# Performance work log

Hardware: AMD Instinct MI355X
Metric: run time of the kernel (lower is better)

The kernel has to match this reference:

```python
import jax, jax.numpy as jnp
import numpy as np

V = 256       # num_variables
D = 512       # hidden_dim
B = 1024      # batch


def setup_inputs() -> dict:
    key = jax.random.key(0)
    ks = jax.random.split(key, 8)
    s1 = 1.0 / np.sqrt(V + 1)
    s2 = 1.0 / np.sqrt(D)
    return {
        "x": jax.random.normal(ks[0], (B, V), dtype=jnp.float32),
        "adjacency": jax.random.normal(ks[1], (V, V), dtype=jnp.float32),
        "W1": jax.random.normal(ks[2], (V, D, V + 1), dtype=jnp.float32) * s1,
        "b1": jax.random.normal(ks[3], (V, D), dtype=jnp.float32) * s1,
        "W2": jax.random.normal(ks[4], (V, D, D), dtype=jnp.float32) * s2,
        "b2": jax.random.normal(ks[5], (V, D), dtype=jnp.float32) * s2,
        "W3": jax.random.normal(ks[6], (V, D), dtype=jnp.float32) * s2,
        "b3": jax.random.normal(ks[7], (V,), dtype=jnp.float32) * s2,
    }


def reference(x, adjacency, W1, b1, W2, b2, W3, b3):
    # weighted_x[b, i] = (x @ A.T)[b, i]
    wx = x @ adjacency.T  # [B, V]
    # combined input for variable i: cat([x, wx[:, i:i+1]]) -> width V+1
    # build [B, V, V+1] by broadcasting x across the variable axis
    x_b = jnp.broadcast_to(x[:, None, :], (x.shape[0], V, V))
    comb = jnp.concatenate([x_b, wx[:, :, None]], axis=-1)  # [B, V, V+1]
    # per-variable 3-layer MLP, batched over the variable axis i
    h1 = jax.nn.relu(jnp.einsum('bij,idj->bid', comb, W1) + b1)   # [B, V, D]
    h2 = jax.nn.relu(jnp.einsum('bid,ied->bie', h1, W2) + b2)     # [B, V, D]
    out = jnp.einsum('bid,id->bi', h2, W3) + b3                   # [B, V]
    return out
```

## Files before the change

### kernel.cpp

```cpp
#include <hip/hip_runtime.h>
#include <hip/hip_bf16.h>
#include <stdint.h>

#define VNUM 256
#define DNUM 512
#define BNUM 1024

typedef __attribute__((ext_vector_type(8))) short bf16x8;
typedef __attribute__((ext_vector_type(4))) float f32x4;

__device__ __forceinline__ uint16_t f2bf(float f) {
    uint32_t u = __float_as_uint(f);
    uint32_t r = (u + 0x7FFFu + ((u >> 16) & 1u)) >> 16;
    return (uint16_t)r;
}

__device__ __forceinline__ void gl_lds16(const void* g, void* l) {
    __builtin_amdgcn_global_load_lds(
        (const __attribute__((address_space(1))) uint32_t*)g,
        (__attribute__((address_space(3))) uint32_t*)l, 16, 0, 0);
}

__global__ __launch_bounds__(256) void wx_kernel(const float* __restrict__ x,
                                                 const float* __restrict__ adj,
                                                 float* __restrict__ wx) {
    __shared__ float xs[64][36];
    __shared__ float as_[64][36];
    const int b0 = blockIdx.x * 64, i0 = blockIdx.y * 64;
    const int t = threadIdx.x;
    const int tx = t & 15, ty = t >> 4;
    const int lr = t >> 2, lk = (t & 3) * 8;
    float c[4][4] = {};
    for (int k0 = 0; k0 < 256; k0 += 32) {
        __syncthreads();
        *(float4*)&xs[lr][lk]      = *(const float4*)&x[(size_t)(b0 + lr) * VNUM + k0 + lk];
        *(float4*)&xs[lr][lk + 4]  = *(const float4*)&x[(size_t)(b0 + lr) * VNUM + k0 + lk + 4];
        *(float4*)&as_[lr][lk]     = *(const float4*)&adj[(size_t)(i0 + lr) * VNUM + k0 + lk];
        *(float4*)&as_[lr][lk + 4] = *(const float4*)&adj[(size_t)(i0 + lr) * VNUM + k0 + lk + 4];
        __syncthreads();
        #pragma unroll
        for (int kk = 0; kk < 32; kk++) {
            float xv[4], av[4];
            #pragma unroll
            for (int a = 0; a < 4; a++) xv[a] = xs[ty + a * 16][kk];
            #pragma unroll
            for (int b = 0; b < 4; b++) av[b] = as_[tx + b * 16][kk];
            #pragma unroll
            for (int a = 0; a < 4; a++)
                #pragma unroll
                for (int b = 0; b < 4; b++) c[a][b] += xv[a] * av[b];
        }
    }
    #pragma unroll
    for (int a = 0; a < 4; a++)
        #pragma unroll
        for (int b = 0; b < 4; b++)
            wx[(size_t)(b0 + ty + a * 16) * VNUM + i0 + tx + b * 16] = c[a][b];
}

__global__ __launch_bounds__(256) void xcvt_kernel(const float* __restrict__ x,
                                                   uint16_t* __restrict__ xbf) {
    const int idx = (blockIdx.x * 256 + threadIdx.x) * 4;
    float4 v = *(const float4*)&x[idx];
    uint32_t p0 = (uint32_t)f2bf(v.x) | ((uint32_t)f2bf(v.y) << 16);
    uint32_t p1 = (uint32_t)f2bf(v.z) | ((uint32_t)f2bf(v.w) << 16);
    *(uint2*)&xbf[idx] = make_uint2(p0, p1);
}

__global__ __launch_bounds__(256) void w1cvt_kernel(const float* __restrict__ W1,
                                                    uint16_t* __restrict__ W1bf,
                                                    float* __restrict__ w1last) {
    const size_t idx = (size_t)blockIdx.x * 256 + threadIdx.x;
    const size_t row = idx >> 8;
    const int    k   = (int)(idx & 255);
    const float* src = W1 + row * 257;
    W1bf[idx] = f2bf(src[k]);
    if (k == 0) w1last[row] = src[256];
}

__global__ __launch_bounds__(256) void w2cvt_kernel(const float* __restrict__ W2,
                                                    uint16_t* __restrict__ W2bf) {
    const size_t idx = ((size_t)blockIdx.x * 256 + threadIdx.x) * 4;
    float4 v = *(const float4*)&W2[idx];
    uint32_t p0 = (uint32_t)f2bf(v.x) | ((uint32_t)f2bf(v.y) << 16);
    uint32_t p1 = (uint32_t)f2bf(v.z) | ((uint32_t)f2bf(v.w) << 16);
    *(uint2*)&W2bf[idx] = make_uint2(p0, p1);
}

__global__ __launch_bounds__(256) void gemm1_kernel(const uint16_t* __restrict__ xbf,
                                                    const float* __restrict__ wx,
                                                    const uint16_t* __restrict__ W1bf,
                                                    const float* __restrict__ w1last,
                                                    const float* __restrict__ b1,
                                                    uint16_t* __restrict__ h1) {
    const int b0 = blockIdx.x * 128;
    const int d0 = blockIdx.y * 128;
    const int ci = blockIdx.z;
    const int i  = ci;

    __shared__ __align__(16) uint16_t As[128 * 32];
    __shared__ __align__(16) uint16_t Bs[128 * 32];
    __shared__ float wxs[128], w1ls[128], b1s[128];

    const int t = threadIdx.x;
    const int w = t >> 6, l = t & 63;
    const int wm = w >> 1, wn = w & 1;
    const int q = l >> 4, lo = l & 15;

    if (t < 128) {
        wxs[t] = wx[(size_t)(b0 + t) * VNUM + i];
        b1s[t] = b1[(size_t)i * DNUM + d0 + t];
    } else {
        int tt = t - 128;
        w1ls[tt] = w1last[(size_t)i * DNUM + d0 + tt];
    }

    f32x4 acc[4][4];
    #pragma unroll
    for (int a = 0; a < 4; a++)
        #pragma unroll
        for (int b = 0; b < 4; b++) { f32x4 z = {0.f, 0.f, 0.f, 0.f}; acc[a][b] = z; }

    const int c_  = w * 64 + l;
    const int rA  = c_ >> 2,        kA = (c_ & 3) ^ ((rA >> 2) & 0);

    const uint16_t* Abase = xbf;
    const uint16_t* Bbase = W1bf + (size_t)i * DNUM * 256;

    for (int k0 = 0; k0 < 256; k0 += 32) {
        __syncthreads();
        #pragma unroll
        for (int p = 0; p < 2; p++) {
            int c  = p * 256 + w * 64 + l;
            int r  = c >> 2, k2 = c & 3;
            int gk2 = k2 ^ ((r >> 1) & 3);
            gl_lds16(Abase + (size_t)(b0 + r) * 256 + k0 + gk2 * 8,
                     &As[(p * 256 + w * 64) * 8]);
        }
        #pragma unroll
        for (int p = 0; p < 2; p++) {
            int c  = p * 256 + w * 64 + l;
            int r  = c >> 2, k2 = c & 3;
            int gk2 = k2 ^ ((r >> 1) & 3);
            gl_lds16(Bbase + (size_t)(d0 + r) * 256 + k0 + gk2 * 8,
                     &Bs[(p * 256 + w * 64) * 8]);
        }
        __syncthreads();
        bf16x8 af[4], bfr[4];
        #pragma unroll
        for (int mt = 0; mt < 4; mt++) {
            int m = wm * 64 + mt * 16 + lo;
            int slot = q ^ ((m >> 1) & 3);
            af[mt] = *(const bf16x8*)&As[m * 32 + slot * 8];
        }
        #pragma unroll
        for (int nt = 0; nt < 4; nt++) {
            int n = wn * 64 + nt * 16 + lo;
            int slot = q ^ ((n >> 1) & 3);
            bfr[nt] = *(const bf16x8*)&Bs[n * 32 + slot * 8];
        }
        #pragma unroll
        for (int mt = 0; mt < 4; mt++)
            #pragma unroll
            for (int nt = 0; nt < 4; nt++)
                acc[mt][nt] = __builtin_amdgcn_mfma_f32_16x16x32_bf16(af[mt], bfr[nt], acc[mt][nt], 0, 0, 0);
    }
    (void)rA; (void)kA;

    #pragma unroll
    for (int mt = 0; mt < 4; mt++) {
        #pragma unroll
        for (int reg = 0; reg < 4; reg++) {
            int row = wm * 64 + mt * 16 + q * 4 + reg;
            size_t rowbase = ((size_t)ci * BNUM + b0 + row) * DNUM + d0;
            float wxv = wxs[row];
            #pragma unroll
            for (int nt = 0; nt < 4; nt++) {
                int col = wn * 64 + nt * 16 + lo;
                float v = acc[mt][nt][reg] + wxv * w1ls[col] + b1s[col];
                v = fmaxf(v, 0.f);
                h1[rowbase + col] = f2bf(v);
            }
        }
    }
}

__global__ __launch_bounds__(256) void gemm2_kernel(const uint16_t* __restrict__ h1,
                                                    const uint16_t* __restrict__ W2bf,
                                                    const float* __restrict__ b2,
                                                    const float* __restrict__ W3,
                                                    const float* __restrict__ b3,
                                                    float* __restrict__ out) {
    const int b0 = blockIdx.x * 128;
    const int e0 = blockIdx.y * 128;
    const int ci = blockIdx.z;
    const int i  = ci;

    __shared__ __align__(16) uint16_t As[128 * 32];
    __shared__ __align__(16) uint16_t Bs[128 * 32];
    __shared__ float b2s[128], w3s[128];
    __shared__ float red[2][128];

    const int t = threadIdx.x;
    const int w = t >> 6, l = t & 63;
    const int wm = w >> 1, wn = w & 1;
    const int q = l >> 4, lo = l & 15;

    if (t < 128) b2s[t] = b2[(size_t)i * DNUM + e0 + t];
    else         w3s[t - 128] = W3[(size_t)i * DNUM + e0 + (t - 128)];

    f32x4 acc[4][4];
    #pragma unroll
    for (int a = 0; a < 4; a++)
        #pragma unroll
        for (int b = 0; b < 4; b++) { f32x4 z = {0.f, 0.f, 0.f, 0.f}; acc[a][b] = z; }

    const uint16_t* Abase = h1 + (size_t)ci * BNUM * DNUM;
    const uint16_t* Bbase = W2bf + (size_t)i * DNUM * DNUM;

    for (int k0 = 0; k0 < 512; k0 += 32) {
        __syncthreads();
        #pragma unroll
        for (int p = 0; p < 2; p++) {
            int c  = p * 256 + w * 64 + l;
            int r  = c >> 2, k2 = c & 3;
            int gk2 = k2 ^ ((r >> 1) & 3);
            gl_lds16(Abase + (size_t)(b0 + r) * DNUM + k0 + gk2 * 8,
                     &As[(p * 256 + w * 64) * 8]);
        }
        #pragma unroll
        for (int p = 0; p < 2; p++) {
            int c  = p * 256 + w * 64 + l;
            int r  = c >> 2, k2 = c & 3;
            int gk2 = k2 ^ ((r >> 1) & 3);
            gl_lds16(Bbase + (size_t)(e0 + r) * DNUM + k0 + gk2 * 8,
                     &Bs[(p * 256 + w * 64) * 8]);
        }
        __syncthreads();
        bf16x8 af[4], bfr[4];
        #pragma unroll
        for (int mt = 0; mt < 4; mt++) {
            int m = wm * 64 + mt * 16 + lo;
            int slot = q ^ ((m >> 1) & 3);
            af[mt] = *(const bf16x8*)&As[m * 32 + slot * 8];
        }
        #pragma unroll
        for (int nt = 0; nt < 4; nt++) {
            int n = wn * 64 + nt * 16 + lo;
            int slot = q ^ ((n >> 1) & 3);
            bfr[nt] = *(const bf16x8*)&Bs[n * 32 + slot * 8];
        }
        #pragma unroll
        for (int mt = 0; mt < 4; mt++)
            #pragma unroll
            for (int nt = 0; nt < 4; nt++)
                acc[mt][nt] = __builtin_amdgcn_mfma_f32_16x16x32_bf16(af[mt], bfr[nt], acc[mt][nt], 0, 0, 0);
    }

    float rs[4][4];
    #pragma unroll
    for (int mt = 0; mt < 4; mt++) {
        #pragma unroll
        for (int reg = 0; reg < 4; reg++) {
            float v = 0.f;
            #pragma unroll
            for (int nt = 0; nt < 4; nt++) {
                int col = wn * 64 + nt * 16 + lo;
                float h = acc[mt][nt][reg] + b2s[col];
                h = fmaxf(h, 0.f);
                v += h * w3s[col];
            }
            v += __shfl_xor(v, 1, 64);
            v += __shfl_xor(v, 2, 64);
            v += __shfl_xor(v, 4, 64);
            v += __shfl_xor(v, 8, 64);
            rs[mt][reg] = v;
        }
    }
    if (lo == 0) {
        #pragma unroll
        for (int mt = 0; mt < 4; mt++)
            #pragma unroll
            for (int reg = 0; reg < 4; reg++) {
                int row = wm * 64 + mt * 16 + q * 4 + reg;
                red[wn][row] = rs[mt][reg];
            }
    }
    __syncthreads();
    if (t < 128) {
        float v = red[0][t] + red[1][t];
        if (e0 == 0) v += b3[i];
        atomicAdd(&out[(size_t)(b0 + t) * VNUM + i], v);
    }
}

extern "C" void kernel_launch(void* const* d_in, const int* in_sizes, int n_in,
                              void* d_out, int out_size, void* d_ws, size_t ws_size,
                              hipStream_t stream) {
    const float* x   = (const float*)d_in[0];
    const float* adj = (const float*)d_in[1];
    const float* W1  = (const float*)d_in[2];
    const float* b1  = (const float*)d_in[3];
    const float* W2  = (const float*)d_in[4];
    const float* b2  = (const float*)d_in[5];
    const float* W3  = (const float*)d_in[6];
    const float* b3  = (const float*)d_in[7];
    float* out = (float*)d_out;

    char* ws = (char*)d_ws;
    float*    wx     = (float*)ws;
    uint16_t* xbf    = (uint16_t*)(ws + (1 << 20));
    float*    w1last = (float*)(ws + (1 << 20) + (1 << 19));
    char*     p      = ws + (2 << 20);
    uint16_t* W1bf   = (uint16_t*)p;
    p += (size_t)VNUM * DNUM * 256 * 2;
    uint16_t* W2bf   = (uint16_t*)p;
    p += (size_t)VNUM * DNUM * DNUM * 2;
    uint16_t* h1     = (uint16_t*)p;

    hipMemsetAsync(d_out, 0, (size_t)BNUM * VNUM * sizeof(float), stream);
    wx_kernel<<<dim3(16, 4), 256, 0, stream>>>(x, adj, wx);
    xcvt_kernel<<<256, 256, 0, stream>>>(x, xbf);
    w1cvt_kernel<<<(VNUM * DNUM * 256) / 256, 256, 0, stream>>>(W1, W1bf, w1last);
    w2cvt_kernel<<<(VNUM * DNUM * DNUM) / (4 * 256), 256, 0, stream>>>(W2, W2bf);
    gemm1_kernel<<<dim3(8, 4, VNUM), 256, 0, stream>>>(xbf, wx, W1bf, w1last, b1, h1);
    gemm2_kernel<<<dim3(8, 4, VNUM), 256, 0, stream>>>(h1, W2bf, b2, W3, b3, out);
}
```

Before: 891.7 us.

## Fuse both MLP GEMMs into one kernel keeping h1 in shared memory

Replaces the separate gemm1 and gemm2 kernels with a single fused kernel. Each block handles one variable and 64 batch rows, computes the full h1 tile into LDS, then runs the second GEMM and the W3 reduction without writing h1 to global memory. This removes the global h1 round trip (256×1024×512 bf16), the output memset and the atomics. Weight slices are double-buffered per wave with explicit vmcnt waits. The W1 conversion kernel is also vectorised to read float4. The cost is that each block re-streams the full W1 and W2 slice for its variable, since 16 batch tiles each reread the weights, and large LDS use limits occupancy.

```diff
diff --git a/kernel.cpp b/kernel.cpp
--- a/kernel.cpp
+++ b/kernel.cpp
@@ -1,5 +1,4 @@
 #include <hip/hip_runtime.h>
-#include <hip/hip_bf16.h>
 #include <stdint.h>
 
 #define VNUM 256
@@ -19,6 +18,17 @@
     __builtin_amdgcn_global_load_lds(
         (const __attribute__((address_space(1))) uint32_t*)g,
         (__attribute__((address_space(3))) uint32_t*)l, 16, 0, 0);
+}
+
+__device__ __forceinline__ void stage_slice(const uint16_t* __restrict__ gbase,
+                                            int kstride, uint16_t* lbase, int l) {
+    #pragma unroll
+    for (int p = 0; p < 4; p++) {
+        const int c = p * 64 + l;
+        const int r = c >> 2, k2 = c & 3;
+        const int gk2 = k2 ^ ((r >> 1) & 3);
+        gl_lds16(gbase + (size_t)r * kstride + gk2 * 8, lbase + p * 512);
+    }
 }
 
 __global__ __launch_bounds__(256) void wx_kernel(const float* __restrict__ x,
@@ -70,12 +80,18 @@
 __global__ __launch_bounds__(256) void w1cvt_kernel(const float* __restrict__ W1,
                                                     uint16_t* __restrict__ W1bf,
                                                     float* __restrict__ w1last) {
-    const size_t idx = (size_t)blockIdx.x * 256 + threadIdx.x;
-    const size_t row = idx >> 8;
-    const int    k   = (int)(idx & 255);
-    const float* src = W1 + row * 257;
-    W1bf[idx] = f2bf(src[k]);
-    if (k == 0) w1last[row] = src[256];
+    const uint32_t i4   = blockIdx.x * 256 + threadIdx.x;
+    const uint32_t base = i4 * 4;
+    float4 v = *(const float4*)&W1[base];
+    float vv[4] = {v.x, v.y, v.z, v.w};
+    #pragma unroll
+    for (int j = 0; j < 4; j++) {
+        uint32_t pos = base + j;
+        uint32_t row = pos / 257u;
+        uint32_t k   = pos - row * 257u;
+        if (k == 256u) w1last[row] = vv[j];
+        else           W1bf[(size_t)row * 256 + k] = f2bf(vv[j]);
+    }
 }
 
 __global__ __launch_bounds__(256) void w2cvt_kernel(const float* __restrict__ W2,
@@ -87,33 +103,49 @@
     *(uint2*)&W2bf[idx] = make_uint2(p0, p1);
 }
 
-__global__ __launch_bounds__(256) void gemm1_kernel(const uint16_t* __restrict__ xbf,
-                                                    const float* __restrict__ wx,
-                                                    const uint16_t* __restrict__ W1bf,
-                                                    const float* __restrict__ w1last,
-                                                    const float* __restrict__ b1,
-                                                    uint16_t* __restrict__ h1) {
-    const int b0 = blockIdx.x * 128;
-    const int d0 = blockIdx.y * 128;
-    const int ci = blockIdx.z;
-    const int i  = ci;
-
-    __shared__ __align__(16) uint16_t As[128 * 32];
-    __shared__ __align__(16) uint16_t Bs[128 * 32];
-    __shared__ float wxs[128], w1ls[128], b1s[128];
-
-    const int t = threadIdx.x;
-    const int w = t >> 6, l = t & 63;
-    const int wm = w >> 1, wn = w & 1;
-    const int q = l >> 4, lo = l & 15;
-
-    if (t < 128) {
-        wxs[t] = wx[(size_t)(b0 + t) * VNUM + i];
-        b1s[t] = b1[(size_t)i * DNUM + d0 + t];
-    } else {
-        int tt = t - 128;
-        w1ls[tt] = w1last[(size_t)i * DNUM + d0 + tt];
-    }
+__global__ __launch_bounds__(512, 2) void fused_kernel(
+        const uint16_t* __restrict__ xbf, const float* __restrict__ wx,
+        const uint16_t* __restrict__ W1bf, const float* __restrict__ w1last,
+        const float* __restrict__ b1, const uint16_t* __restrict__ W2bf,
+        const float* __restrict__ b2, const float* __restrict__ W3,
+        const float* __restrict__ b3, float* __restrict__ out) {
+
+    __shared__ __align__(16) uint16_t h1s[16 * 64 * 32];
+    __shared__ __align__(16) uint16_t Ws[8 * 4096];
+    __shared__ float w1ls[DNUM], b1s[DNUM], b2s[DNUM], w3s[DNUM];
+    __shared__ float wxs[64];
+    __shared__ float red[8][64];
+
+    const int bid = blockIdx.x;
+    const int swz = (bid & 7) * 512 + (bid >> 3);
+    const int i   = swz >> 4;
+    const int b0  = (swz & 15) * 64;
+
+    const int t  = threadIdx.x;
+    const int w  = t >> 6, l = t & 63;
+    const int lo = l & 15, q = l >> 4;
+    const int sA = (lo >> 1) & 3;
+
+    w1ls[t] = w1last[(size_t)i * DNUM + t];
+    b1s[t]  = b1[(size_t)i * DNUM + t];
+    b2s[t]  = b2[(size_t)i * DNUM + t];
+    w3s[t]  = W3[(size_t)i * DNUM + t];
+    if (t < 64) wxs[t] = wx[(size_t)(b0 + t) * VNUM + i];
+
+    #pragma unroll
+    for (int p = 0; p < 4; p++) {
+        const int cb = p * 512 + w * 64;
+        const int c  = cb + l;
+        const int kt = c >> 8, cc = c & 255;
+        const int r = cc >> 2, k2 = cc & 3;
+        const int gk2 = k2 ^ ((r >> 1) & 3);
+        gl_lds16(xbf + (size_t)(b0 + r) * VNUM + kt * 32 + gk2 * 8, &h1s[cb * 8]);
+    }
+    __syncthreads();
+
+    uint16_t* myW = &Ws[w * 4096];
+    const uint16_t* W1b = W1bf + ((size_t)i * DNUM + w * 64) * 256;
+    const uint16_t* W2b = W2bf + ((size_t)i * DNUM + w * 64) * 512;
 
     f32x4 acc[4][4];
     #pragma unroll
@@ -121,143 +153,83 @@
         #pragma unroll
         for (int b = 0; b < 4; b++) { f32x4 z = {0.f, 0.f, 0.f, 0.f}; acc[a][b] = z; }
 
-    const int c_  = w * 64 + l;
-    const int rA  = c_ >> 2,        kA = (c_ & 3) ^ ((rA >> 2) & 0);
-
-    const uint16_t* Abase = xbf;
-    const uint16_t* Bbase = W1bf + (size_t)i * DNUM * 256;
-
-    for (int k0 = 0; k0 < 256; k0 += 32) {
-        __syncthreads();
-        #pragma unroll
-        for (int p = 0; p < 2; p++) {
-            int c  = p * 256 + w * 64 + l;
-            int r  = c >> 2, k2 = c & 3;
-            int gk2 = k2 ^ ((r >> 1) & 3);
-            gl_lds16(Abase + (size_t)(b0 + r) * 256 + k0 + gk2 * 8,
-                     &As[(p * 256 + w * 64) * 8]);
+    stage_slice(W1b, 256, myW, l);
+    #pragma unroll
+    for (int kt = 0; kt < 8; kt++) {
+        const int cur = (kt & 1) * 2048;
+        if (kt < 7) stage_slice(W1b + (kt + 1) * 32, 256, myW + (((kt & 1) ^ 1) * 2048), l);
+        if (kt < 7) asm volatile("s_waitcnt vmcnt(4)" ::: "memory");
+        else        asm volatile("s_waitcnt vmcnt(0)" ::: "memory");
+        bf16x8 af[4], bx[4];
+        #pragma unroll
+        for (int mt = 0; mt < 4; mt++)
+            af[mt] = *(const bf16x8*)&myW[cur + (mt * 16 + lo) * 32 + (q ^ sA) * 8];
+        #pragma unroll
+        for (int nt = 0; nt < 4; nt++)
+            bx[nt] = *(const bf16x8*)&h1s[kt * 2048 + (nt * 16 + lo) * 32 + (q ^ sA) * 8];
+        __builtin_amdgcn_s_setprio(1);
+        #pragma unroll
+        for (int mt = 0; mt < 4; mt++)
+            #pragma unroll
+            for (int nt = 0; nt < 4; nt++)
+                acc[mt][nt] = __builtin_amdgcn_mfma_f32_16x16x32_bf16(af[mt], bx[nt], acc[mt][nt], 0, 0, 0);
+        __builtin_amdgcn_s_setprio(0);
+        __builtin_amdgcn_sched_barrier(0);
+    }
+
+    __syncthreads();
+
+    #pragma unroll
+    for (int mt = 0; mt < 4; mt++) {
+        const int dbase = w * 64 + mt * 16 + q * 4;
+        const int ktile = dbase >> 5;
+        const int dk    = dbase & 31;
+        const int slot  = dk >> 3;
+        const int sub   = dk & 7;
+        #pragma unroll
+        for (int nt = 0; nt < 4; nt++) {
+            const int b = nt * 16 + lo;
+            const float wxv = wxs[b];
+            float v0 = acc[mt][nt][0] + wxv * w1ls[dbase + 0] + b1s[dbase + 0];
+            float v1 = acc[mt][nt][1] + wxv * w1ls[dbase + 1] + b1s[dbase + 1];
+            float v2 = acc[mt][nt][2] + wxv * w1ls[dbase + 2] + b1s[dbase + 2];
+            float v3 = acc[mt][nt][3] + wxv * w1ls[dbase + 3] + b1s[dbase + 3];
+            uint32_t lo32 = (uint32_t)f2bf(fmaxf(v0, 0.f)) | ((uint32_t)f2bf(fmaxf(v1, 0.f)) << 16);
+            uint32_t hi32 = (uint32_t)f2bf(fmaxf(v2, 0.f)) | ((uint32_t)f2bf(fmaxf(v3, 0.f)) << 16);
+            const int sslot = slot ^ sA;
+            *(uint2*)&h1s[ktile * 2048 + b * 32 + sslot * 8 + sub] = make_uint2(lo32, hi32);
         }
-        #pragma unroll
-        for (int p = 0; p < 2; p++) {
-            int c  = p * 256 + w * 64 + l;
-            int r  = c >> 2, k2 = c & 3;
-            int gk2 = k2 ^ ((r >> 1) & 3);
-            gl_lds16(Bbase + (size_t)(d0 + r) * 256 + k0 + gk2 * 8,
-                     &Bs[(p * 256 + w * 64) * 8]);
-        }
-        __syncthreads();
-        bf16x8 af[4], bfr[4];
-        #pragma unroll
-        for (int mt = 0; mt < 4; mt++) {
-            int m = wm * 64 + mt * 16 + lo;
-            int slot = q ^ ((m >> 1) & 3);
-            af[mt] = *(const bf16x8*)&As[m * 32 + slot * 8];
-        }
-        #pragma unroll
-        for (int nt = 0; nt < 4; nt++) {
-            int n = wn * 64 + nt * 16 + lo;
-            int slot = q ^ ((n >> 1) & 3);
-            bfr[nt] = *(const bf16x8*)&Bs[n * 32 + slot * 8];
-        }
+    }
+    #pragma unroll
+    for (int a = 0; a < 4; a++)
+        #pragma unroll
+        for (int b = 0; b < 4; b++) { f32x4 z = {0.f, 0.f, 0.f, 0.f}; acc[a][b] = z; }
+    __syncthreads();
+
+    stage_slice(W2b, 512, myW, l);
+    #pragma unroll
+    for (int kt = 0; kt < 16; kt++) {
+        const int cur = (kt & 1) * 2048;
+        if (kt < 15) stage_slice(W2b + (kt + 1) * 32, 512, myW + (((kt & 1) ^ 1) * 2048), l);
+        if (kt < 15) asm volatile("s_waitcnt vmcnt(4)" ::: "memory");
+        else         asm volatile("s_waitcnt vmcnt(0)" ::: "memory");
+        bf16x8 ah[4], bw[4];
+        #pragma unroll
+        for (int mt = 0; mt < 4; mt++)
+            ah[mt] = *(const bf16x8*)&h1s[kt * 2048 + (mt * 16 + lo) * 32 + (q ^ sA) * 8];
+        #pragma unroll
+        for (int nt = 0; nt < 4; nt++)
+            bw[nt] = *(const bf16x8*)&myW[cur + (nt * 16 + lo) * 32 + (q ^ sA) * 8];
+        __builtin_amdgcn_s_setprio(1);
         #pragma unroll
         for (int mt = 0; mt < 4; mt++)
             #pragma unroll
             for (int nt = 0; nt < 4; nt++)
-                acc[mt][nt] = __builtin_amdgcn_mfma_f32_16x16x32_bf16(af[mt], bfr[nt], acc[mt][nt], 0, 0, 0);
-    }
-    (void)rA; (void)kA;
-
-    #pragma unroll
-    for (int mt = 0; mt < 4; mt++) {
-        #pragma unroll
-        for (int reg = 0; reg < 4; reg++) {
-            int row = wm * 64 + mt * 16 + q * 4 + reg;
-            size_t rowbase = ((size_t)ci * BNUM + b0 + row) * DNUM + d0;
-            float wxv = wxs[row];
-            #pragma unroll
-            for (int nt = 0; nt < 4; nt++) {
-                int col = wn * 64 + nt * 16 + lo;
-                float v = acc[mt][nt][reg] + wxv * w1ls[col] + b1s[col];
-                v = fmaxf(v, 0.f);
-                h1[rowbase + col] = f2bf(v);
-            }
-        }
-    }
-}
-
-__global__ __launch_bounds__(256) void gemm2_kernel(const uint16_t* __restrict__ h1,
-                                                    const uint16_t* __restrict__ W2bf,
-                                                    const float* __restrict__ b2,
-                                                    const float* __restrict__ W3,
-                                                    const float* __restrict__ b3,
-                                                    float* __restrict__ out) {
-    const int b0 = blockIdx.x * 128;
-    const int e0 = blockIdx.y * 128;
-    const int ci = blockIdx.z;
-    const int i  = ci;
-
-    __shared__ __align__(16) uint16_t As[128 * 32];
-    __shared__ __align__(16) uint16_t Bs[128 * 32];
-    __shared__ float b2s[128], w3s[128];
-    __shared__ float red[2][128];
-
-    const int t = threadIdx.x;
-    const int w = t >> 6, l = t & 63;
-    const int wm = w >> 1, wn = w & 1;
-    const int q = l >> 4, lo = l & 15;
-
-    if (t < 128) b2s[t] = b2[(size_t)i * DNUM + e0 + t];
-    else         w3s[t - 128] = W3[(size_t)i * DNUM + e0 + (t - 128)];
-
-    f32x4 acc[4][4];
-    #pragma unroll
-    for (int a = 0; a < 4; a++)
-        #pragma unroll
-        for (int b = 0; b < 4; b++) { f32x4 z = {0.f, 0.f, 0.f, 0.f}; acc[a][b] = z; }
-
-    const uint16_t* Abase = h1 + (size_t)ci * BNUM * DNUM;
-    const uint16_t* Bbase = W2bf + (size_t)i * DNUM * DNUM;
-
-    for (int k0 = 0; k0 < 512; k0 += 32) {
-        __syncthreads();
-        #pragma unroll
-        for (int p = 0; p < 2; p++) {
-            int c  = p * 256 + w * 64 + l;
-            int r  = c >> 2, k2 = c & 3;
-            int gk2 = k2 ^ ((r >> 1) & 3);
-            gl_lds16(Abase + (size_t)(b0 + r) * DNUM + k0 + gk2 * 8,
-                     &As[(p * 256 + w * 64) * 8]);
-        }
-        #pragma unroll
-        for (int p = 0; p < 2; p++) {
-            int c  = p * 256 + w * 64 + l;
-            int r  = c >> 2, k2 = c & 3;
-            int gk2 = k2 ^ ((r >> 1) & 3);
-            gl_lds16(Bbase + (size_t)(e0 + r) * DNUM + k0 + gk2 * 8,
-                     &Bs[(p * 256 + w * 64) * 8]);
-        }
-        __syncthreads();
-        bf16x8 af[4], bfr[4];
-        #pragma unroll
-        for (int mt = 0; mt < 4; mt++) {
-            int m = wm * 64 + mt * 16 + lo;
-            int slot = q ^ ((m >> 1) & 3);
-            af[mt] = *(const bf16x8*)&As[m * 32 + slot * 8];
-        }
-        #pragma unroll
-        for (int nt = 0; nt < 4; nt++) {
-            int n = wn * 64 + nt * 16 + lo;
-            int slot = q ^ ((n >> 1) & 3);
-            bfr[nt] = *(const bf16x8*)&Bs[n * 32 + slot * 8];
-        }
-        #pragma unroll
-        for (int mt = 0; mt < 4; mt++)
-            #pragma unroll
-            for (int nt = 0; nt < 4; nt++)
-                acc[mt][nt] = __builtin_amdgcn_mfma_f32_16x16x32_bf16(af[mt], bfr[nt], acc[mt][nt], 0, 0, 0);
-    }
-
-    float rs[4][4];
+                acc[mt][nt] = __builtin_amdgcn_mfma_f32_16x16x32_bf16(ah[mt], bw[nt], acc[mt][nt], 0, 0, 0);
+        __builtin_amdgcn_s_setprio(0);
+        __builtin_amdgcn_sched_barrier(0);
+    }
+
     #pragma unroll
     for (int mt = 0; mt < 4; mt++) {
         #pragma unroll
@@ -265,32 +237,24 @@
             float v = 0.f;
             #pragma unroll
             for (int nt = 0; nt < 4; nt++) {
-                int col = wn * 64 + nt * 16 + lo;
-                float h = acc[mt][nt][reg] + b2s[col];
+                const int e = w * 64 + nt * 16 + lo;
+                float h = acc[mt][nt][reg] + b2s[e];
                 h = fmaxf(h, 0.f);
-                v += h * w3s[col];
+                v += h * w3s[e];
             }
             v += __shfl_xor(v, 1, 64);
             v += __shfl_xor(v, 2, 64);
             v += __shfl_xor(v, 4, 64);
             v += __shfl_xor(v, 8, 64);
-            rs[mt][reg] = v;
+            if (lo == 0) red[w][mt * 16 + q * 4 + reg] = v;
         }
     }
-    if (lo == 0) {
-        #pragma unroll
-        for (int mt = 0; mt < 4; mt++)
-            #pragma unroll
-            for (int reg = 0; reg < 4; reg++) {
-                int row = wm * 64 + mt * 16 + q * 4 + reg;
-                red[wn][row] = rs[mt][reg];
-            }
-    }
-    __syncthreads();
-    if (t < 128) {
-        float v = red[0][t] + red[1][t];
-        if (e0 == 0) v += b3[i];
-        atomicAdd(&out[(size_t)(b0 + t) * VNUM + i], v);
+    __syncthreads();
+    if (t < 64) {
+        float v = b3[i];
+        #pragma unroll
+        for (int ww = 0; ww < 8; ww++) v += red[ww][t];
+        out[(size_t)(b0 + t) * VNUM + i] = v;
     }
 }
 
@@ -315,14 +279,10 @@
     uint16_t* W1bf   = (uint16_t*)p;
     p += (size_t)VNUM * DNUM * 256 * 2;
     uint16_t* W2bf   = (uint16_t*)p;
-    p += (size_t)VNUM * DNUM * DNUM * 2;
-    uint16_t* h1     = (uint16_t*)p;
-
-    hipMemsetAsync(d_out, 0, (size_t)BNUM * VNUM * sizeof(float), stream);
+
     wx_kernel<<<dim3(16, 4), 256, 0, stream>>>(x, adj, wx);
     xcvt_kernel<<<256, 256, 0, stream>>>(x, xbf);
-    w1cvt_kernel<<<(VNUM * DNUM * 256) / 256, 256, 0, stream>>>(W1, W1bf, w1last);
-    w2cvt_kernel<<<(VNUM * DNUM * DNUM) / (4 * 256), 256, 0, stream>>>(W2, W2bf);
-    gemm1_kernel<<<dim3(8, 4, VNUM), 256, 0, stream>>>(xbf, wx, W1bf, w1last, b1, h1);
-    gemm2_kernel<<<dim3(8, 4, VNUM), 256, 0, stream>>>(h1, W2bf, b2, W3, b3, out);
-}
+    w1cvt_kernel<<<(VNUM * DNUM * 257) / (4 * 256), 256, 0, stream>>>(W1, W1bf, w1last);
+    w2cvt_kernel<<<(size_t)(VNUM * DNUM * DNUM) / (4 * 256), 256, 0, stream>>>(W2, W2bf);
+    fused_kernel<<<4096, 512, 0, stream>>>(xbf, wx, W1bf, w1last, b1, W2bf, b2, W3, b3, out);
+}
```

Measured after the change: 837.0 us. -6.1%, faster.
